# Kernel optimization log

Measured on AMD Instinct MI355X. Metric: run time of the kernel, lower is better.

Reference implementation:

```python
import jax, jax.numpy as jnp
import numpy as np

INV_SCALE = 1.0 / (0.5 * 9)  # module's inv_scale_factor; qk is DIVIDED by this (i.e. * 4.5)


def setup_inputs() -> dict:
    key0 = jax.random.key(0)
    ks = jax.random.split(key0, 8)
    B, Sq, Sk, D, Dv = 8, 2048, 2048, 128, 256
    return {
        "query": jax.random.normal(ks[0], (B, Sq, D), dtype=jnp.float32),
        "key": jax.random.normal(ks[1], (B, Sk, D), dtype=jnp.float32),
        "value": jax.random.normal(ks[2], (B, Sk, Dv), dtype=jnp.float32),
        "mask": jax.random.normal(ks[3], (B, Sq, Sk), dtype=jnp.float32),
        # Linear weights stored torch-style as [out_features, in_features]
        "W0": jax.random.normal(ks[4], (D, D), dtype=jnp.float32) * (1.0 / np.sqrt(D)),
        "W1": jax.random.normal(ks[5], (D, D), dtype=jnp.float32) * (1.0 / np.sqrt(D)),
        "W2": jax.random.normal(ks[6], (D, Dv), dtype=jnp.float32) * (1.0 / np.sqrt(Dv)),
        "Wout": jax.random.normal(ks[7], (Dv, D), dtype=jnp.float32) * (1.0 / np.sqrt(D)),
    }


def reference(query, key, value, mask, W0, W1, W2, Wout):
    r1 = jnp.einsum("bqd,od->bqo", query, W0)          # [B,Sq,128]
    r2 = jnp.einsum("bkd,od->bko", key, W1)            # [B,Sk,128]
    r3 = jnp.einsum("bkv,ov->bko", value, W2)          # [B,Sk,128]
    qk = jnp.einsum("bqd,bkd->bqk", r1, r2)            # [B,Sq,Sk]
    scaled_qk = qk / INV_SCALE
    softmax_qk = jax.nn.softmax(scaled_qk, axis=-1)
    # dropout is identity in eval mode (deterministic reference)
    v1 = jnp.einsum("bqk,bko->bqo", softmax_qk, r3)    # [B,Sq,128]
    v2 = jnp.einsum("bqo,vo->bqv", v1, Wout)           # [B,Sq,256]
    output = v2 + jnp.einsum("bqk,bkv->bqv", mask, value)
    return output
```

## Files before the change

kernel.cpp:

```cpp
#include <hip/hip_runtime.h>
#include <cstdint>

typedef __attribute__((ext_vector_type(8))) __bf16 bf16x8;
typedef __attribute__((ext_vector_type(4))) __bf16 bf16x4;
typedef __attribute__((ext_vector_type(4))) float f32x4;

#define MFMA16(a, b, c) __builtin_amdgcn_mfma_f32_16x16x32_bf16((a), (b), (c), 0, 0, 0)
#define WAITV(N) asm volatile("s_waitcnt vmcnt(" #N ")" ::: "memory")

static constexpr int SEQ = 2048;
static constexpr int DV = 256;
static constexpr float QK_SCALE = 4.5f;

__device__ __forceinline__ bf16x4 cvt4(float4 v) {
    bf16x4 y;
    y[0] = (__bf16)v.x; y[1] = (__bf16)v.y; y[2] = (__bf16)v.z; y[3] = (__bf16)v.w;
    return y;
}

__device__ __forceinline__ void gl_lds16(const void* g, void* l) {
    __builtin_amdgcn_global_load_lds((const __attribute__((address_space(1))) uint32_t*)g,
                                     (__attribute__((address_space(3))) uint32_t*)l, 16, 0, 0);
}

template <int K, int TRANS>
__device__ __forceinline__ void proj_body(const float* __restrict__ X,
                                          const float* __restrict__ W,
                                          __bf16* __restrict__ out,
                                          float outScale, int m0, char* smem) {
    auto ldsX = (__bf16(*)[136])smem;
    auto ldsW = (__bf16(*)[136])(smem + 64 * 136 * 2);

    const int t = threadIdx.x;
    const int w = t >> 6, l = t & 63, lrow = l & 15, lq = l >> 4;

    f32x4 acc[8];
#pragma unroll
    for (int i = 0; i < 8; ++i) acc[i] = f32x4{0.f, 0.f, 0.f, 0.f};

#pragma unroll
    for (int kh = 0; kh < K / 128; ++kh) {
        if (kh) __syncthreads();
#pragma unroll
        for (int i = 0; i < 8; ++i) {
            int idx = t + i * 256;
            int r = idx >> 5, c4 = idx & 31;
            float4 v = *(const float4*)(X + (size_t)(m0 + r) * K + kh * 128 + c4 * 4);
            *(bf16x4*)&ldsX[r][c4 * 4] = cvt4(v);
        }
#pragma unroll
        for (int i = 0; i < 16; ++i) {
            int idx = t + i * 256;
            int r = idx >> 5, c4 = idx & 31;
            float4 v = *(const float4*)(W + (size_t)r * K + kh * 128 + c4 * 4);
            *(bf16x4*)&ldsW[r][c4 * 4] = cvt4(v);
        }
        __syncthreads();

        bf16x8 aA[4];
#pragma unroll
        for (int kc = 0; kc < 4; ++kc)
            aA[kc] = *(const bf16x8*)((const char*)&ldsX[w * 16 + lrow][0] + kc * 64 + lq * 16);
#pragma unroll
        for (int nt = 0; nt < 8; ++nt) {
#pragma unroll
            for (int kc = 0; kc < 4; ++kc) {
                bf16x8 bB = *(const bf16x8*)((const char*)&ldsW[nt * 16 + lrow][0] + kc * 64 + lq * 16);
                acc[nt] = MFMA16(aA[kc], bB, acc[nt]);
            }
        }
    }

#pragma unroll
    for (int nt = 0; nt < 8; ++nt) {
        if (TRANS) {
            int gm = m0 + w * 16 + lq * 4;
            int b = gm >> 11, s = gm & 2047;
            int col = nt * 16 + lrow;
            int kt = s >> 5, s32 = s & 31;
            int slot = (s32 >> 3) ^ ((col >> 1) & 3);
            bf16x4 y;
#pragma unroll
            for (int j = 0; j < 4; ++j) y[j] = (__bf16)(acc[nt][j] * outScale);
            *(bf16x4*)(out + (((size_t)b * 64 + kt) * 128 + col) * 32 + slot * 8 + (s32 & 7)) = y;
        } else {
#pragma unroll
            for (int j = 0; j < 4; ++j) {
                int gm = m0 + w * 16 + lq * 4 + j;
                int col = nt * 16 + lrow;
                out[(size_t)gm * 128 + col] = (__bf16)(acc[nt][j] * outScale);
            }
        }
    }
}

__device__ __forceinline__ void vt_body(const float* __restrict__ V,
                                        __bf16* __restrict__ vt, int wg, char* smem) {
    auto tile = (__bf16(*)[72])smem;
    const int t = threadIdx.x;
    const int b = wg >> 7, by = (wg >> 5) & 3, bxx = wg & 31;
    const int s0 = bxx * 64, v0 = by * 64;
#pragma unroll
    for (int i = 0; i < 4; ++i) {
        int idx = t + i * 256;
        int r = idx >> 4, c4 = idx & 15;
        float4 x = *(const float4*)(V + ((size_t)b * SEQ + s0 + r) * DV + v0 + c4 * 4);
        *(bf16x4*)&tile[r][c4 * 4] = cvt4(x);
    }
    __syncthreads();
#pragma unroll
    for (int i = 0; i < 4; ++i) {
        int idx = t + i * 256;
        int vv = idx >> 4, c4 = idx & 15;
        bf16x4 y;
        y[0] = tile[c4 * 4 + 0][vv]; y[1] = tile[c4 * 4 + 1][vv];
        y[2] = tile[c4 * 4 + 2][vv]; y[3] = tile[c4 * 4 + 3][vv];
        int v = v0 + vv;
        int kt = (s0 >> 5) + (c4 >> 3);
        int slot = ((c4 >> 1) & 3) ^ ((v >> 1) & 3);
        *(bf16x4*)(vt + (((size_t)b * 64 + kt) * 256 + v) * 32 + slot * 8 + (c4 & 1) * 4) = y;
    }
}

__global__ __launch_bounds__(256) void k_pre(const float* __restrict__ q,
                                             const float* __restrict__ k,
                                             const float* __restrict__ v,
                                             const float* __restrict__ W0,
                                             const float* __restrict__ W1,
                                             const float* __restrict__ W2,
                                             const float* __restrict__ Wout,
                                             const float* __restrict__ mask,
                                             __bf16* __restrict__ r1s,
                                             __bf16* __restrict__ r2b,
                                             __bf16* __restrict__ r3t,
                                             __bf16* __restrict__ vtb,
                                             __bf16* __restrict__ wob,
                                             __bf16* __restrict__ maskb) {
    __shared__ __align__(16) char smem[52224];
    const int bx = blockIdx.x;
    if (bx < 256) {
        proj_body<128, 0>(q, W0, r1s, QK_SCALE, bx * 64, smem);
    } else if (bx < 512) {
        proj_body<128, 0>(k, W1, r2b, 1.0f, (bx - 256) * 64, smem);
    } else if (bx < 768) {
        proj_body<256, 1>(v, W2, r3t, 1.0f, (bx - 512) * 64, smem);
    } else if (bx < 1792) {
        vt_body(v, vtb, bx - 768, smem);
    } else if (bx < 1824) {
        int i = (bx - 1792) * 256 + threadIdx.x;
        if (i < 8192) {
            float4 x = *(const float4*)(Wout + (size_t)i * 4);
            *(bf16x4*)(wob + (size_t)i * 4) = cvt4(x);
        }
    } else {
        const size_t N = (size_t)8 * 2048 * 2048;
        const size_t stride = (size_t)1024 * 256 * 8;
        size_t i = ((size_t)(bx - 1824) * 256 + threadIdx.x) * 8;
        for (; i < N; i += stride) {
            float4 a = *(const float4*)(mask + i);
            float4 b2 = *(const float4*)(mask + i + 4);
            bf16x8 o;
            o[0] = (__bf16)a.x; o[1] = (__bf16)a.y; o[2] = (__bf16)a.z; o[3] = (__bf16)a.w;
            o[4] = (__bf16)b2.x; o[5] = (__bf16)b2.y; o[6] = (__bf16)b2.z; o[7] = (__bf16)b2.w;
            *(bf16x8*)(maskb + i) = o;
        }
    }
}

__global__ __launch_bounds__(256) void k_flash(const __bf16* __restrict__ r1s,
                                               const __bf16* __restrict__ r2,
                                               const __bf16* __restrict__ r3p,
                                               __bf16* __restrict__ v1p,
                                               float* __restrict__ ml) {
    __shared__ __align__(16) __bf16 r2s[2][32 * 128];
    __shared__ __align__(16) __bf16 r3s[2][128 * 32];
    __shared__ __bf16 plds[4][16][48];

    const int t = threadIdx.x;
    const int bx = (int)((blockIdx.x & 7) * 128 + (blockIdx.x >> 3));
    const int b = bx >> 7, rem = bx & 127, q0 = (rem >> 2) * 64, kh = rem & 3;
    const int w = t >> 6, l = t & 63, lrow = l & 15, lq = l >> 4;

    const __bf16* r1b = r1s + (size_t)b * SEQ * 128;
    const __bf16* r2b = r2 + (size_t)b * SEQ * 128 + (size_t)kh * 512 * 128;
    const __bf16* r3b = r3p + (size_t)b * 64 * 128 * 32 + (size_t)kh * 16 * 128 * 32;

    bf16x8 aQ[4];
    {
        const __bf16* p = r1b + (size_t)(q0 + w * 16 + lrow) * 128 + lq * 8;
#pragma unroll
        for (int kc = 0; kc < 4; ++kc) aQ[kc] = *(const bf16x8*)(p + kc * 32);
    }

    const __bf16* p_r2[2];
    const __bf16* p_r3[2];
#pragma unroll
    for (int q1 = 0; q1 < 2; ++q1) {
        int r = 8 * w + 4 * q1 + (l >> 4);
        int c = (l & 15) ^ (r & 15);
        p_r2[q1] = r2b + (size_t)r * 128 + c * 8;
        p_r3[q1] = r3b + (size_t)(2 * w + q1) * 512 + l * 8;
    }

    auto stage = [&](int bi) {
#pragma unroll
        for (int q1 = 0; q1 < 2; ++q1) {
            gl_lds16(p_r2[q1], &r2s[bi][(2 * w + q1) * 512]);
            gl_lds16(p_r3[q1], &r3s[bi][(2 * w + q1) * 512]);
            p_r2[q1] += 32 * 128;
            p_r3[q1] += 128 * 32;
        }
    };

    f32x4 acc[8];
#pragma unroll
    for (int i = 0; i < 8; ++i) acc[i] = f32x4{0.f, 0.f, 0.f, 0.f};
    float mrow[4] = {-INFINITY, -INFINITY, -INFINITY, -INFINITY};
    float lsum[4] = {0.f, 0.f, 0.f, 0.f};

    stage(0);
    for (int it = 0; it < 16; ++it) {
        if (it + 1 < 16) stage((it + 1) & 1);
        if (it < 15) { WAITV(4); } else { WAITV(0); }
        __builtin_amdgcn_s_barrier();
        __builtin_amdgcn_sched_barrier(0);
        const __bf16* R2 = &r2s[it & 1][0];
        const __bf16* R3 = &r3s[it & 1][0];

        f32x4 sc[2];
#pragma unroll
        for (int ct = 0; ct < 2; ++ct) {
            f32x4 s = f32x4{0.f, 0.f, 0.f, 0.f};
#pragma unroll
            for (int kc = 0; kc < 4; ++kc) {
                int p = (kc * 4 + lq) ^ lrow;
                bf16x8 bb = *(const bf16x8*)&R2[(ct * 16 + lrow) * 128 + p * 8];
                s = MFMA16(aQ[kc], bb, s);
            }
            sc[ct] = s;
        }

        float pm[4], al[4];
#pragma unroll
        for (int j = 0; j < 4; ++j) pm[j] = fmaxf(sc[0][j], sc[1][j]);
#pragma unroll
        for (int off = 1; off <= 8; off <<= 1)
#pragma unroll
            for (int j = 0; j < 4; ++j) pm[j] = fmaxf(pm[j], __shfl_xor(pm[j], off, 64));
#pragma unroll
        for (int j = 0; j < 4; ++j) {
            float mn = fmaxf(mrow[j], pm[j]);
            al[j] = __expf(mrow[j] - mn);
            mrow[j] = mn;
        }
        float pr[2][4];
#pragma unroll
        for (int ct = 0; ct < 2; ++ct)
#pragma unroll
            for (int j = 0; j < 4; ++j)
                pr[ct][j] = __expf(sc[ct][j] - mrow[j]);
#pragma unroll
        for (int j = 0; j < 4; ++j)
            lsum[j] = lsum[j] * al[j] + pr[0][j] + pr[1][j];
#pragma unroll
        for (int ot = 0; ot < 8; ++ot)
#pragma unroll
            for (int j = 0; j < 4; ++j) acc[ot][j] *= al[j];

#pragma unroll
        for (int ct = 0; ct < 2; ++ct)
#pragma unroll
            for (int j = 0; j < 4; ++j)
                plds[w][lq * 4 + j][ct * 16 + lrow] = (__bf16)pr[ct][j];
        __builtin_amdgcn_s_waitcnt(0xc07f);
        bf16x8 pA = *(const bf16x8*)&plds[w][lrow][lq * 8];

#pragma unroll
        for (int ot = 0; ot < 8; ++ot) {
            int p = lq ^ ((lrow >> 1) & 3);
            bf16x8 bb = *(const bf16x8*)&R3[(ot * 16 + lrow) * 32 + p * 8];
            acc[ot] = MFMA16(pA, bb, acc[ot]);
        }
        __builtin_amdgcn_s_barrier();
    }

#pragma unroll
    for (int off = 1; off <= 8; off <<= 1)
#pragma unroll
        for (int j = 0; j < 4; ++j) lsum[j] += __shfl_xor(lsum[j], off, 64);

    __bf16* vp = v1p + (size_t)kh * 8 * SEQ * 128;
#pragma unroll
    for (int ot = 0; ot < 8; ++ot)
#pragma unroll
        for (int j = 0; j < 4; ++j) {
            int q = q0 + w * 16 + lq * 4 + j;
            float v = acc[ot][j] / lsum[j];
            vp[((size_t)b * SEQ + q) * 128 + ot * 16 + lrow] = (__bf16)v;
        }
    if (lrow == 0) {
#pragma unroll
        for (int j = 0; j < 4; ++j) {
            size_t row = (size_t)b * SEQ + q0 + w * 16 + lq * 4 + j;
            ml[((size_t)kh * 8 * SEQ + row) * 2 + 0] = mrow[j];
            ml[((size_t)kh * 8 * SEQ + row) * 2 + 1] = lsum[j];
        }
    }
}

__global__ __launch_bounds__(512, 2) void k_out(const __bf16* __restrict__ maskb,
                                                const __bf16* __restrict__ vtp,
                                                const __bf16* __restrict__ v1p,
                                                const float* __restrict__ ml,
                                                const __bf16* __restrict__ wob,
                                                float* __restrict__ out) {
    __shared__ __align__(16) __bf16 vbuf[3][256 * 32];
    __shared__ __align__(16) __bf16 mbuf[4][64 * 64];

    const int t = threadIdx.x;
    const int bid = (int)((blockIdx.x & 7) * 32 + (blockIdx.x >> 3));
    const int m0 = bid * 64;
    const int b = m0 >> 11, q0 = m0 & 2047;
    const int w = t >> 6, l = t & 63, lrow = l & 15, lq = l >> 4;
    const int rg = w & 3, ch = w >> 2;

    f32x4 acc[8];
#pragma unroll
    for (int i = 0; i < 8; ++i) acc[i] = f32x4{0.f, 0.f, 0.f, 0.f};

    const __bf16* vsrc[4];
    const __bf16* msrc[2];
    if (w < 4) {
#pragma unroll
        for (int i = 0; i < 4; ++i)
            vsrc[i] = vtp + (size_t)b * 64 * 8192 + (w * 4 + i) * 512 + l * 8;
    } else {
        const int m = w - 4;
        int c = (l & 7) ^ (l >> 3);
#pragma unroll
        for (int s = 0; s < 2; ++s)
            msrc[s] = maskb + ((size_t)(b * 2048 + q0 + 16 * m + 8 * s + (l >> 3))) * 2048 + c * 8;
    }

    if (w < 4) {
#pragma unroll
        for (int kt = 0; kt < 2; ++kt)
#pragma unroll
            for (int i = 0; i < 4; ++i)
                gl_lds16(vsrc[i] + (size_t)kt * 8192, &vbuf[kt][(w * 4 + i) * 512]);
    } else {
        const int m = w - 4;
#pragma unroll
        for (int e = 0; e < 2; ++e)
#pragma unroll
            for (int s = 0; s < 2; ++s)
                gl_lds16(msrc[s] + (size_t)e * 64, &mbuf[e][(16 * m + 8 * s) * 64]);
    }

    for (int it = 0; it < 64; ++it) {
        if (w >= 4) {
            const int m = w - 4;
            if ((it & 1) == 0) {
                int en = (it >> 1) + 2;
                if (en <= 31) {
                    gl_lds16(msrc[0] + (size_t)en * 64, &mbuf[en & 3][(16 * m) * 64]);
                    gl_lds16(msrc[1] + (size_t)en * 64, &mbuf[en & 3][(16 * m + 8) * 64]);
                }
                if (it <= 58) { WAITV(4); } else if (it == 60) { WAITV(2); } else { WAITV(0); }
            }
        } else {
            if (it < 63) { WAITV(4); } else { WAITV(0); }
        }
        __builtin_amdgcn_s_barrier();
        __builtin_amdgcn_sched_barrier(0);
        if (w < 4 && it + 2 < 64) {
            int kt = it + 2;
#pragma unroll
            for (int i = 0; i < 4; ++i)
                gl_lds16(vsrc[i] + (size_t)kt * 8192, &vbuf[kt % 3][(w * 4 + i) * 512]);
        }
        __builtin_amdgcn_sched_barrier(0);

        const __bf16* Mb = &mbuf[(it >> 1) & 3][0];
        const __bf16* V = &vbuf[it % 3][0];
        const int h = it & 1;
        bf16x8 aM = *(const bf16x8*)&Mb[(rg * 16 + lrow) * 64 + (((h * 4 + lq) ^ (lrow & 7)) * 8)];

        const int pv = lq ^ ((lrow >> 1) & 3);
#pragma unroll
        for (int vt8 = 0; vt8 < 8; ++vt8) {
            bf16x8 bb = *(const bf16x8*)&V[(ch * 128 + vt8 * 16 + lrow) * 32 + pv * 8];
            acc[vt8] = MFMA16(aM, bb, acc[vt8]);
        }
    }

    const int NROW = 8 * SEQ;
    const int row = m0 + rg * 16 + lrow;
    float mp[4], lp[4];
    float mm = -INFINITY;
#pragma unroll
    for (int p = 0; p < 4; ++p) {
        mp[p] = ml[((size_t)p * NROW + row) * 2 + 0];
        lp[p] = ml[((size_t)p * NROW + row) * 2 + 1];
        mm = fmaxf(mm, mp[p]);
    }
    float wp[4], wsum = 0.f;
#pragma unroll
    for (int p = 0; p < 4; ++p) { wp[p] = lp[p] * __expf(mp[p] - mm); wsum += wp[p]; }
    float inv = 1.f / wsum;
#pragma unroll
    for (int p = 0; p < 4; ++p) wp[p] *= inv;

    bf16x8 aV[4];
#pragma unroll
    for (int oc = 0; oc < 4; ++oc) {
        float s[8];
#pragma unroll
        for (int j = 0; j < 8; ++j) s[j] = 0.f;
#pragma unroll
        for (int p = 0; p < 4; ++p) {
            bf16x8 x = *(const bf16x8*)(v1p + ((size_t)p * NROW + row) * 128 + oc * 32 + lq * 8);
#pragma unroll
            for (int j = 0; j < 8; ++j) s[j] += wp[p] * (float)x[j];
        }
#pragma unroll
        for (int j = 0; j < 8; ++j) aV[oc][j] = (__bf16)s[j];
    }
#pragma unroll
    for (int vt8 = 0; vt8 < 8; ++vt8) {
#pragma unroll
        for (int oc = 0; oc < 4; ++oc) {
            bf16x8 bb = *(const bf16x8*)(wob + (size_t)(ch * 128 + vt8 * 16 + lrow) * 128 + oc * 32 + lq * 8);
            acc[vt8] = MFMA16(aV[oc], bb, acc[vt8]);
        }
    }

#pragma unroll
    for (int vt8 = 0; vt8 < 8; ++vt8)
#pragma unroll
        for (int j = 0; j < 4; ++j) {
            int gq = m0 + rg * 16 + lq * 4 + j;
            out[(size_t)gq * 256 + ch * 128 + vt8 * 16 + lrow] = acc[vt8][j];
        }
}

extern "C" void kernel_launch(void* const* d_in, const int* in_sizes, int n_in,
                              void* d_out, int out_size, void* d_ws, size_t ws_size,
                              hipStream_t stream) {
    const float* q    = (const float*)d_in[0];
    const float* k    = (const float*)d_in[1];
    const float* v    = (const float*)d_in[2];
    const float* mask = (const float*)d_in[3];
    const float* W0   = (const float*)d_in[4];
    const float* W1   = (const float*)d_in[5];
    const float* W2   = (const float*)d_in[6];
    const float* Wout = (const float*)d_in[7];
    float* out = (float*)d_out;

    char* ws = (char*)d_ws;
    __bf16* r1s = (__bf16*)(ws);
    __bf16* r2b = (__bf16*)(ws + (4ull << 20));
    __bf16* r3t = (__bf16*)(ws + (8ull << 20));
    __bf16* vtb = (__bf16*)(ws + (12ull << 20));
    __bf16* wob = (__bf16*)(ws + (20ull << 20));
    float*  mlb = (float*)(ws + (20ull << 20) + (512ull << 10));
    __bf16* v1p = (__bf16*)(ws + (21ull << 20));
    __bf16* mkb = (__bf16*)(ws + (37ull << 20));

    k_pre<<<2848, 256, 0, stream>>>(q, k, v, W0, W1, W2, Wout, mask,
                                    r1s, r2b, r3t, vtb, wob, mkb);
    k_flash<<<1024, 256, 0, stream>>>(r1s, r2b, r3t, v1p, mlb);
    k_out<<<256, 512, 0, stream>>>(mkb, vtb, v1p, mlb, wob, out);
}
```

Measured before the change: 345.2 us.

## Interleave mask conversion blocks in pre-kernel and widen output kernel to 1024 threads

The pre-kernel now interleaves mask fp32-to-bf16 conversion blocks with the projection blocks and unrolls the conversion 16-deep per thread, so conversion memory traffic overlaps with compute-bound projection work instead of running in a trailing tail. The output kernel doubles its threads to 16 waves: each wave now holds half the accumulators (4 column tiles) and issues half the async loads, with wait counts adjusted to match. This is meant to add latency hiding and parallelism in the mask@V stage. The cost is extra LDS-read traffic and barrier participants per block, plus more registers held for the unrolled loads in the conversion path.

```diff
diff --git a/kernel.cpp b/kernel.cpp
--- a/kernel.cpp
+++ b/kernel.cpp
@@ -137,7 +137,34 @@
                                              __bf16* __restrict__ wob,
                                              __bf16* __restrict__ maskb) {
     __shared__ __align__(16) char smem[52224];
-    const int bx = blockIdx.x;
+    const int bx0 = blockIdx.x;
+    int bx; bool is_cvt;
+    if (bx0 < 2048) { is_cvt = (bx0 & 1); bx = bx0 >> 1; }
+    else            { is_cvt = false; bx = 1024 + (bx0 - 2048); }
+
+    if (is_cvt) {
+        const size_t stride = (size_t)1024 * 256 * 8;
+        size_t base = ((size_t)bx * 256 + threadIdx.x) * 8;
+#pragma unroll
+        for (int g = 0; g < 4; ++g) {
+            float4 a[4], b2[4];
+            size_t i0 = base + (size_t)g * 4 * stride;
+#pragma unroll
+            for (int u = 0; u < 4; ++u) {
+                a[u]  = *(const float4*)(mask + i0 + (size_t)u * stride);
+                b2[u] = *(const float4*)(mask + i0 + (size_t)u * stride + 4);
+            }
+#pragma unroll
+            for (int u = 0; u < 4; ++u) {
+                bf16x8 o;
+                o[0] = (__bf16)a[u].x; o[1] = (__bf16)a[u].y; o[2] = (__bf16)a[u].z; o[3] = (__bf16)a[u].w;
+                o[4] = (__bf16)b2[u].x; o[5] = (__bf16)b2[u].y; o[6] = (__bf16)b2[u].z; o[7] = (__bf16)b2[u].w;
+                *(bf16x8*)(maskb + i0 + (size_t)u * stride) = o;
+            }
+        }
+        return;
+    }
+
     if (bx < 256) {
         proj_body<128, 0>(q, W0, r1s, QK_SCALE, bx * 64, smem);
     } else if (bx < 512) {
@@ -146,23 +173,11 @@
         proj_body<256, 1>(v, W2, r3t, 1.0f, (bx - 512) * 64, smem);
     } else if (bx < 1792) {
         vt_body(v, vtb, bx - 768, smem);
-    } else if (bx < 1824) {
+    } else {
         int i = (bx - 1792) * 256 + threadIdx.x;
         if (i < 8192) {
             float4 x = *(const float4*)(Wout + (size_t)i * 4);
             *(bf16x4*)(wob + (size_t)i * 4) = cvt4(x);
-        }
-    } else {
-        const size_t N = (size_t)8 * 2048 * 2048;
-        const size_t stride = (size_t)1024 * 256 * 8;
-        size_t i = ((size_t)(bx - 1824) * 256 + threadIdx.x) * 8;
-        for (; i < N; i += stride) {
-            float4 a = *(const float4*)(mask + i);
-            float4 b2 = *(const float4*)(mask + i + 4);
-            bf16x8 o;
-            o[0] = (__bf16)a.x; o[1] = (__bf16)a.y; o[2] = (__bf16)a.z; o[3] = (__bf16)a.w;
-            o[4] = (__bf16)b2.x; o[5] = (__bf16)b2.y; o[6] = (__bf16)b2.z; o[7] = (__bf16)b2.w;
-            *(bf16x8*)(maskb + i) = o;
         }
     }
 }
@@ -308,12 +323,12 @@
     }
 }
 
-__global__ __launch_bounds__(512, 2) void k_out(const __bf16* __restrict__ maskb,
-                                                const __bf16* __restrict__ vtp,
-                                                const __bf16* __restrict__ v1p,
-                                                const float* __restrict__ ml,
-                                                const __bf16* __restrict__ wob,
-                                                float* __restrict__ out) {
+__global__ __launch_bounds__(1024) void k_out(const __bf16* __restrict__ maskb,
+                                              const __bf16* __restrict__ vtp,
+                                              const __bf16* __restrict__ v1p,
+                                              const float* __restrict__ ml,
+                                              const __bf16* __restrict__ wob,
+                                              float* __restrict__ out) {
     __shared__ __align__(16) __bf16 vbuf[3][256 * 32];
     __shared__ __align__(16) __bf16 mbuf[4][64 * 64];
 
@@ -322,62 +337,55 @@
     const int m0 = bid * 64;
     const int b = m0 >> 11, q0 = m0 & 2047;
     const int w = t >> 6, l = t & 63, lrow = l & 15, lq = l >> 4;
-    const int rg = w & 3, ch = w >> 2;
-
-    f32x4 acc[8];
-#pragma unroll
-    for (int i = 0; i < 8; ++i) acc[i] = f32x4{0.f, 0.f, 0.f, 0.f};
-
-    const __bf16* vsrc[4];
-    const __bf16* msrc[2];
-    if (w < 4) {
-#pragma unroll
-        for (int i = 0; i < 4; ++i)
-            vsrc[i] = vtp + (size_t)b * 64 * 8192 + (w * 4 + i) * 512 + l * 8;
+    const int rg = w & 3, cg = w >> 2;
+
+    f32x4 acc[4];
+#pragma unroll
+    for (int i = 0; i < 4; ++i) acc[i] = f32x4{0.f, 0.f, 0.f, 0.f};
+
+    const __bf16* vsrc[2];
+    const __bf16* msrc = nullptr;
+    if (w < 8) {
+#pragma unroll
+        for (int i = 0; i < 2; ++i)
+            vsrc[i] = vtp + (size_t)b * 64 * 8192 + (w * 2 + i) * 512 + l * 8;
     } else {
-        const int m = w - 4;
+        const int m = w - 8;
         int c = (l & 7) ^ (l >> 3);
-#pragma unroll
-        for (int s = 0; s < 2; ++s)
-            msrc[s] = maskb + ((size_t)(b * 2048 + q0 + 16 * m + 8 * s + (l >> 3))) * 2048 + c * 8;
-    }
-
-    if (w < 4) {
+        msrc = maskb + ((size_t)(b * 2048 + q0 + 8 * m + (l >> 3))) * 2048 + c * 8;
+    }
+
+    if (w < 8) {
 #pragma unroll
         for (int kt = 0; kt < 2; ++kt)
 #pragma unroll
-            for (int i = 0; i < 4; ++i)
-                gl_lds16(vsrc[i] + (size_t)kt * 8192, &vbuf[kt][(w * 4 + i) * 512]);
+            for (int i = 0; i < 2; ++i)
+                gl_lds16(vsrc[i] + (size_t)kt * 8192, &vbuf[kt][(w * 2 + i) * 512]);
     } else {
-        const int m = w - 4;
+        const int m = w - 8;
 #pragma unroll
         for (int e = 0; e < 2; ++e)
-#pragma unroll
-            for (int s = 0; s < 2; ++s)
-                gl_lds16(msrc[s] + (size_t)e * 64, &mbuf[e][(16 * m + 8 * s) * 64]);
+            gl_lds16(msrc + (size_t)e * 64, &mbuf[e][m * 512]);
     }
 
     for (int it = 0; it < 64; ++it) {
-        if (w >= 4) {
-            const int m = w - 4;
+        if (w >= 8) {
+            const int m = w - 8;
             if ((it & 1) == 0) {
                 int en = (it >> 1) + 2;
-                if (en <= 31) {
-                    gl_lds16(msrc[0] + (size_t)en * 64, &mbuf[en & 3][(16 * m) * 64]);
-                    gl_lds16(msrc[1] + (size_t)en * 64, &mbuf[en & 3][(16 * m + 8) * 64]);
-                }
-                if (it <= 58) { WAITV(4); } else if (it == 60) { WAITV(2); } else { WAITV(0); }
+                if (en <= 31) gl_lds16(msrc + (size_t)en * 64, &mbuf[en & 3][m * 512]);
+                if (it <= 58) { WAITV(2); } else if (it == 60) { WAITV(1); } else { WAITV(0); }
             }
         } else {
-            if (it < 63) { WAITV(4); } else { WAITV(0); }
+            if (it < 63) { WAITV(2); } else { WAITV(0); }
         }
         __builtin_amdgcn_s_barrier();
         __builtin_amdgcn_sched_barrier(0);
-        if (w < 4 && it + 2 < 64) {
+        if (w < 8 && it + 2 < 64) {
             int kt = it + 2;
 #pragma unroll
-            for (int i = 0; i < 4; ++i)
-                gl_lds16(vsrc[i] + (size_t)kt * 8192, &vbuf[kt % 3][(w * 4 + i) * 512]);
+            for (int i = 0; i < 2; ++i)
+                gl_lds16(vsrc[i] + (size_t)kt * 8192, &vbuf[kt % 3][(w * 2 + i) * 512]);
         }
         __builtin_amdgcn_sched_barrier(0);
 
@@ -388,8 +396,8 @@
 
         const int pv = lq ^ ((lrow >> 1) & 3);
 #pragma unroll
-        for (int vt8 = 0; vt8 < 8; ++vt8) {
-            bf16x8 bb = *(const bf16x8*)&V[(ch * 128 + vt8 * 16 + lrow) * 32 + pv * 8];
+        for (int vt8 = 0; vt8 < 4; ++vt8) {
+            bf16x8 bb = *(const bf16x8*)&V[(cg * 64 + vt8 * 16 + lrow) * 32 + pv * 8];
             acc[vt8] = MFMA16(aM, bb, acc[vt8]);
         }
     }
@@ -427,20 +435,20 @@
         for (int j = 0; j < 8; ++j) aV[oc][j] = (__bf16)s[j];
     }
 #pragma unroll
-    for (int vt8 = 0; vt8 < 8; ++vt8) {
+    for (int vt8 = 0; vt8 < 4; ++vt8) {
 #pragma unroll
         for (int oc = 0; oc < 4; ++oc) {
-            bf16x8 bb = *(const bf16x8*)(wob + (size_t)(ch * 128 + vt8 * 16 + lrow) * 128 + oc * 32 + lq * 8);
+            bf16x8 bb = *(const bf16x8*)(wob + (size_t)(cg * 64 + vt8 * 16 + lrow) * 128 + oc * 32 + lq * 8);
             acc[vt8] = MFMA16(aV[oc], bb, acc[vt8]);
         }
     }
 
 #pragma unroll
-    for (int vt8 = 0; vt8 < 8; ++vt8)
+    for (int vt8 = 0; vt8 < 4; ++vt8)
 #pragma unroll
         for (int j = 0; j < 4; ++j) {
             int gq = m0 + rg * 16 + lq * 4 + j;
-            out[(size_t)gq * 256 + ch * 128 + vt8 * 16 + lrow] = acc[vt8][j];
+            out[(size_t)gq * 256 + cg * 64 + vt8 * 16 + lrow] = acc[vt8][j];
         }
 }
 
@@ -470,5 +478,5 @@
     k_pre<<<2848, 256, 0, stream>>>(q, k, v, W0, W1, W2, Wout, mask,
                                     r1s, r2b, r3t, vtb, wob, mkb);
     k_flash<<<1024, 256, 0, stream>>>(r1s, r2b, r3t, v1p, mlb);
-    k_out<<<256, 512, 0, stream>>>(mkb, vtb, v1p, mlb, wob, out);
-}
+    k_out<<<256, 1024, 0, stream>>>(mkb, vtb, v1p, mlb, wob, out);
+}
```

New measurement: 352.8 us. 2.2% more time.

## Fuse flash attention with fp32 mask-value GEMM and split out epilogue kernel

Applied to the files above, without the earlier changes.

Removes the separate mask fp32-to-bf16 conversion pass. The mask@value product now reads the fp32 mask directly and converts it in registers. That GEMM runs in the same launch as the flash-attention blocks, interleaved by block index, so the memory-bound mask streaming overlaps with the compute-bound attention. A new small epilogue kernel merges the split-K partial softmax results, applies Wout and accumulates into the output. This adds a read-modify-write of the output and doubles the LDS traffic for the mask in fp32.

```diff
diff --git a/kernel.cpp b/kernel.cpp
--- a/kernel.cpp
+++ b/kernel.cpp
@@ -129,13 +129,11 @@
                                              const float* __restrict__ W1,
                                              const float* __restrict__ W2,
                                              const float* __restrict__ Wout,
-                                             const float* __restrict__ mask,
                                              __bf16* __restrict__ r1s,
                                              __bf16* __restrict__ r2b,
                                              __bf16* __restrict__ r3t,
                                              __bf16* __restrict__ vtb,
-                                             __bf16* __restrict__ wob,
-                                             __bf16* __restrict__ maskb) {
+                                             __bf16* __restrict__ wob) {
     __shared__ __align__(16) char smem[52224];
     const int bx = blockIdx.x;
     if (bx < 256) {
@@ -146,40 +144,30 @@
         proj_body<256, 1>(v, W2, r3t, 1.0f, (bx - 512) * 64, smem);
     } else if (bx < 1792) {
         vt_body(v, vtb, bx - 768, smem);
-    } else if (bx < 1824) {
+    } else {
         int i = (bx - 1792) * 256 + threadIdx.x;
         if (i < 8192) {
             float4 x = *(const float4*)(Wout + (size_t)i * 4);
             *(bf16x4*)(wob + (size_t)i * 4) = cvt4(x);
         }
-    } else {
-        const size_t N = (size_t)8 * 2048 * 2048;
-        const size_t stride = (size_t)1024 * 256 * 8;
-        size_t i = ((size_t)(bx - 1824) * 256 + threadIdx.x) * 8;
-        for (; i < N; i += stride) {
-            float4 a = *(const float4*)(mask + i);
-            float4 b2 = *(const float4*)(mask + i + 4);
-            bf16x8 o;
-            o[0] = (__bf16)a.x; o[1] = (__bf16)a.y; o[2] = (__bf16)a.z; o[3] = (__bf16)a.w;
-            o[4] = (__bf16)b2.x; o[5] = (__bf16)b2.y; o[6] = (__bf16)b2.z; o[7] = (__bf16)b2.w;
-            *(bf16x8*)(maskb + i) = o;
-        }
-    }
-}
-
-__global__ __launch_bounds__(256) void k_flash(const __bf16* __restrict__ r1s,
-                                               const __bf16* __restrict__ r2,
-                                               const __bf16* __restrict__ r3p,
-                                               __bf16* __restrict__ v1p,
-                                               float* __restrict__ ml) {
-    __shared__ __align__(16) __bf16 r2s[2][32 * 128];
-    __shared__ __align__(16) __bf16 r3s[2][128 * 32];
-    __shared__ __bf16 plds[4][16][48];
-
+    }
+}
+
+__device__ __forceinline__ void flash_body(const __bf16* __restrict__ r1s,
+                                           const __bf16* __restrict__ r2,
+                                           const __bf16* __restrict__ r3p,
+                                           __bf16* __restrict__ v1p,
+                                           float* __restrict__ ml,
+                                           int jf, char* smem) {
     const int t = threadIdx.x;
-    const int bx = (int)((blockIdx.x & 7) * 128 + (blockIdx.x >> 3));
-    const int b = bx >> 7, rem = bx & 127, q0 = (rem >> 2) * 64, kh = rem & 3;
-    const int w = t >> 6, l = t & 63, lrow = l & 15, lq = l >> 4;
+    const int unit = t >> 8, t8 = t & 255;
+    const int f = jf * 2 + unit;
+    const int b = f >> 7, rem = f & 127, q0 = (rem >> 2) * 64, kh = rem & 3;
+    const int w = t8 >> 6, l = t8 & 63, lrow = l & 15, lq = l >> 4;
+
+    __bf16* r2s = (__bf16*)(smem + unit * 38912);
+    __bf16* r3s = (__bf16*)(smem + unit * 38912 + 16384);
+    __bf16* plds = (__bf16*)(smem + unit * 38912 + 32768);
 
     const __bf16* r1b = r1s + (size_t)b * SEQ * 128;
     const __bf16* r2b = r2 + (size_t)b * SEQ * 128 + (size_t)kh * 512 * 128;
@@ -205,8 +193,8 @@
     auto stage = [&](int bi) {
 #pragma unroll
         for (int q1 = 0; q1 < 2; ++q1) {
-            gl_lds16(p_r2[q1], &r2s[bi][(2 * w + q1) * 512]);
-            gl_lds16(p_r3[q1], &r3s[bi][(2 * w + q1) * 512]);
+            gl_lds16(p_r2[q1], r2s + bi * 4096 + (2 * w + q1) * 512);
+            gl_lds16(p_r3[q1], r3s + bi * 4096 + (2 * w + q1) * 512);
             p_r2[q1] += 32 * 128;
             p_r3[q1] += 128 * 32;
         }
@@ -224,8 +212,8 @@
         if (it < 15) { WAITV(4); } else { WAITV(0); }
         __builtin_amdgcn_s_barrier();
         __builtin_amdgcn_sched_barrier(0);
-        const __bf16* R2 = &r2s[it & 1][0];
-        const __bf16* R3 = &r3s[it & 1][0];
+        const __bf16* R2 = r2s + (it & 1) * 4096;
+        const __bf16* R3 = r3s + (it & 1) * 4096;
 
         f32x4 sc[2];
 #pragma unroll
@@ -271,9 +259,9 @@
         for (int ct = 0; ct < 2; ++ct)
 #pragma unroll
             for (int j = 0; j < 4; ++j)
-                plds[w][lq * 4 + j][ct * 16 + lrow] = (__bf16)pr[ct][j];
+                plds[w * 768 + (lq * 4 + j) * 48 + ct * 16 + lrow] = (__bf16)pr[ct][j];
         __builtin_amdgcn_s_waitcnt(0xc07f);
-        bf16x8 pA = *(const bf16x8*)&plds[w][lrow][lq * 8];
+        bf16x8 pA = *(const bf16x8*)&plds[w * 768 + lrow * 48 + lq * 8];
 
 #pragma unroll
         for (int ot = 0; ot < 8; ++ot) {
@@ -308,38 +296,39 @@
     }
 }
 
-__global__ __launch_bounds__(512, 2) void k_out(const __bf16* __restrict__ maskb,
-                                                const __bf16* __restrict__ vtp,
-                                                const __bf16* __restrict__ v1p,
-                                                const float* __restrict__ ml,
-                                                const __bf16* __restrict__ wob,
-                                                float* __restrict__ out) {
-    __shared__ __align__(16) __bf16 vbuf[3][256 * 32];
-    __shared__ __align__(16) __bf16 mbuf[4][64 * 64];
+__device__ __forceinline__ void mv_body(const float* __restrict__ mask,
+                                        const __bf16* __restrict__ vtp,
+                                        float* __restrict__ out,
+                                        int jm, char* smem) {
+    float* mbuf = (float*)smem;
+    __bf16* vbuf = (__bf16*)(smem + 32768);
 
     const int t = threadIdx.x;
-    const int bid = (int)((blockIdx.x & 7) * 32 + (blockIdx.x >> 3));
-    const int m0 = bid * 64;
-    const int b = m0 >> 11, q0 = m0 & 2047;
+    const int b = jm & 7, qblk = jm >> 3;
+    const int m0 = b * 2048 + qblk * 32, q0 = qblk * 32;
     const int w = t >> 6, l = t & 63, lrow = l & 15, lq = l >> 4;
-    const int rg = w & 3, ch = w >> 2;
-
-    f32x4 acc[8];
-#pragma unroll
-    for (int i = 0; i < 8; ++i) acc[i] = f32x4{0.f, 0.f, 0.f, 0.f};
+    const int rg = w & 1, ch = w >> 1;
+
+    const int cg = w >> 1;
+
+    f32x4 acc[4];
+#pragma unroll
+    for (int i = 0; i < 4; ++i) acc[i] = f32x4{0.f, 0.f, 0.f, 0.f};
 
     const __bf16* vsrc[4];
-    const __bf16* msrc[2];
+    const float* msrc[2];
     if (w < 4) {
 #pragma unroll
         for (int i = 0; i < 4; ++i)
             vsrc[i] = vtp + (size_t)b * 64 * 8192 + (w * 4 + i) * 512 + l * 8;
     } else {
         const int m = w - 4;
-        int c = (l & 7) ^ (l >> 3);
-#pragma unroll
-        for (int s = 0; s < 2; ++s)
-            msrc[s] = maskb + ((size_t)(b * 2048 + q0 + 16 * m + 8 * s + (l >> 3))) * 2048 + c * 8;
+#pragma unroll
+        for (int s = 0; s < 2; ++s) {
+            int r = 4 * (m * 2 + s) + (l >> 4);
+            int c = (l & 15) ^ (r & 7);
+            msrc[s] = mask + ((size_t)(b * 2048 + q0 + r)) * 2048 + c * 4;
+        }
     }
 
     if (w < 4) {
@@ -347,26 +336,25 @@
         for (int kt = 0; kt < 2; ++kt)
 #pragma unroll
             for (int i = 0; i < 4; ++i)
-                gl_lds16(vsrc[i] + (size_t)kt * 8192, &vbuf[kt][(w * 4 + i) * 512]);
+                gl_lds16(vsrc[i] + (size_t)kt * 8192, vbuf + kt * 8192 + (w * 4 + i) * 512);
     } else {
         const int m = w - 4;
 #pragma unroll
         for (int e = 0; e < 2; ++e)
 #pragma unroll
             for (int s = 0; s < 2; ++s)
-                gl_lds16(msrc[s] + (size_t)e * 64, &mbuf[e][(16 * m + 8 * s) * 64]);
+                gl_lds16(msrc[s] + (size_t)e * 64, mbuf + e * 2048 + (m * 2 + s) * 256);
     }
 
     for (int it = 0; it < 64; ++it) {
         if (w >= 4) {
             const int m = w - 4;
+            if (it <= 59) {
+                int en = (it >> 1) + 2, s = it & 1;
+                gl_lds16(msrc[s] + (size_t)en * 64, mbuf + (en & 3) * 2048 + (m * 2 + s) * 256);
+            }
             if ((it & 1) == 0) {
-                int en = (it >> 1) + 2;
-                if (en <= 31) {
-                    gl_lds16(msrc[0] + (size_t)en * 64, &mbuf[en & 3][(16 * m) * 64]);
-                    gl_lds16(msrc[1] + (size_t)en * 64, &mbuf[en & 3][(16 * m + 8) * 64]);
-                }
-                if (it <= 58) { WAITV(4); } else if (it == 60) { WAITV(2); } else { WAITV(0); }
+                if (it <= 58) { WAITV(3); } else if (it == 60) { WAITV(2); } else { WAITV(0); }
             }
         } else {
             if (it < 63) { WAITV(4); } else { WAITV(0); }
@@ -377,22 +365,67 @@
             int kt = it + 2;
 #pragma unroll
             for (int i = 0; i < 4; ++i)
-                gl_lds16(vsrc[i] + (size_t)kt * 8192, &vbuf[kt % 3][(w * 4 + i) * 512]);
+                gl_lds16(vsrc[i] + (size_t)kt * 8192, vbuf + (kt % 3) * 8192 + (w * 4 + i) * 512);
         }
         __builtin_amdgcn_sched_barrier(0);
 
-        const __bf16* Mb = &mbuf[(it >> 1) & 3][0];
-        const __bf16* V = &vbuf[it % 3][0];
+        const float* Mb = mbuf + ((it >> 1) & 3) * 2048;
+        const __bf16* V = vbuf + (it % 3) * 8192;
         const int h = it & 1;
-        bf16x8 aM = *(const bf16x8*)&Mb[(rg * 16 + lrow) * 64 + (((h * 4 + lq) ^ (lrow & 7)) * 8)];
+        int c0 = (h * 8 + lq * 2) ^ (lrow & 7);
+        int c1 = (h * 8 + lq * 2 + 1) ^ (lrow & 7);
+        float4 f0 = *(const float4*)&Mb[(rg * 16 + lrow) * 64 + c0 * 4];
+        float4 f1 = *(const float4*)&Mb[(rg * 16 + lrow) * 64 + c1 * 4];
+        bf16x8 aM;
+        aM[0] = (__bf16)f0.x; aM[1] = (__bf16)f0.y; aM[2] = (__bf16)f0.z; aM[3] = (__bf16)f0.w;
+        aM[4] = (__bf16)f1.x; aM[5] = (__bf16)f1.y; aM[6] = (__bf16)f1.z; aM[7] = (__bf16)f1.w;
 
         const int pv = lq ^ ((lrow >> 1) & 3);
 #pragma unroll
-        for (int vt8 = 0; vt8 < 8; ++vt8) {
-            bf16x8 bb = *(const bf16x8*)&V[(ch * 128 + vt8 * 16 + lrow) * 32 + pv * 8];
+        for (int vt8 = 0; vt8 < 4; ++vt8) {
+            bf16x8 bb = *(const bf16x8*)&V[(cg * 64 + vt8 * 16 + lrow) * 32 + pv * 8];
             acc[vt8] = MFMA16(aM, bb, acc[vt8]);
         }
     }
+
+#pragma unroll
+    for (int vt8 = 0; vt8 < 4; ++vt8)
+#pragma unroll
+        for (int j = 0; j < 4; ++j) {
+            int gq = m0 + rg * 16 + lq * 4 + j;
+            out[(size_t)gq * 256 + cg * 64 + vt8 * 16 + lrow] = acc[vt8][j];
+        }
+}
+
+__global__ __launch_bounds__(512, 4) void k_fused(const __bf16* __restrict__ r1s,
+                                                  const __bf16* __restrict__ r2b,
+                                                  const __bf16* __restrict__ r3t,
+                                                  __bf16* __restrict__ v1p,
+                                                  float* __restrict__ mlb,
+                                                  const float* __restrict__ mask,
+                                                  const __bf16* __restrict__ vtp,
+                                                  float* __restrict__ out) {
+    __shared__ __align__(16) char smem[81920];
+    const int bx = blockIdx.x;
+    if (((bx >> 8) & 1) == 0) {
+        int jf = (bx < 256) ? bx : bx - 256;
+        flash_body(r1s, r2b, r3t, v1p, mlb, jf, smem);
+    } else {
+        int jm = (bx < 512) ? bx - 256 : bx - 512;
+        if (bx >= 768) jm = bx - 512;
+        else jm = bx - 256;
+        mv_body(mask, vtp, out, jm, smem);
+    }
+}
+
+__global__ __launch_bounds__(256) void k_epi(const __bf16* __restrict__ v1p,
+                                             const float* __restrict__ ml,
+                                             const __bf16* __restrict__ wob,
+                                             float* __restrict__ out) {
+    const int t = threadIdx.x;
+    const int m0 = blockIdx.x * 32;
+    const int w = t >> 6, l = t & 63, lrow = l & 15, lq = l >> 4;
+    const int rg = w & 1, ch = w >> 1;
 
     const int NROW = 8 * SEQ;
     const int row = m0 + rg * 16 + lrow;
@@ -426,6 +459,10 @@
 #pragma unroll
         for (int j = 0; j < 8; ++j) aV[oc][j] = (__bf16)s[j];
     }
+
+    f32x4 acc[8];
+#pragma unroll
+    for (int i = 0; i < 8; ++i) acc[i] = f32x4{0.f, 0.f, 0.f, 0.f};
 #pragma unroll
     for (int vt8 = 0; vt8 < 8; ++vt8) {
 #pragma unroll
@@ -440,7 +477,8 @@
 #pragma unroll
         for (int j = 0; j < 4; ++j) {
             int gq = m0 + rg * 16 + lq * 4 + j;
-            out[(size_t)gq * 256 + ch * 128 + vt8 * 16 + lrow] = acc[vt8][j];
+            size_t o = (size_t)gq * 256 + ch * 128 + vt8 * 16 + lrow;
+            out[o] += acc[vt8][j];
         }
 }
 
@@ -465,10 +503,9 @@
     __bf16* wob = (__bf16*)(ws + (20ull << 20));
     float*  mlb = (float*)(ws + (20ull << 20) + (512ull << 10));
     __bf16* v1p = (__bf16*)(ws + (21ull << 20));
-    __bf16* mkb = (__bf16*)(ws + (37ull << 20));
-
-    k_pre<<<2848, 256, 0, stream>>>(q, k, v, W0, W1, W2, Wout, mask,
-                                    r1s, r2b, r3t, vtb, wob, mkb);
-    k_flash<<<1024, 256, 0, stream>>>(r1s, r2b, r3t, v1p, mlb);
-    k_out<<<256, 512, 0, stream>>>(mkb, vtb, v1p, mlb, wob, out);
-}
+
+    k_pre<<<1824, 256, 0, stream>>>(q, k, v, W0, W1, W2, Wout,
+                                    r1s, r2b, r3t, vtb, wob);
+    k_fused<<<1024, 512, 0, stream>>>(r1s, r2b, r3t, v1p, mlb, mask, vtb, out);
+    k_epi<<<512, 256, 0, stream>>>(v1p, mlb, wob, out);
+}
```

Measured after the change: 324.1 us. -6.1%, faster.
